# Kernel tuning notes

Measured on AMD Instinct MI355X. Metric: run time of the kernel, lower is better.

The kernel has to match this reference:

```python
import jax, jax.numpy as jnp
import numpy as np

DIM = 1024
N_HEADS = 16
HEAD_DIM = DIM // N_HEADS
MAX_SEQ_LEN = 8192
THETA = 10000.0
EPS = 1e-6


def _rope_tables(seq_len):
    freqs = 1.0 / (THETA ** (jnp.arange(0, HEAD_DIM, 2, dtype=jnp.float32) / HEAD_DIM))
    t = jnp.arange(seq_len, dtype=jnp.float32)
    ang = jnp.outer(t, freqs)  # [S, HEAD_DIM/2]
    return jnp.cos(ang), jnp.sin(ang)


def _apply_rope(x, cos, sin):
    # x: [B, H, S, hd]; cos/sin: [S, hd/2] broadcast over B,H
    x1 = x[..., ::2]
    x2 = x[..., 1::2]
    r1 = x1 * cos - x2 * sin
    r2 = x1 * sin + x2 * cos
    # interleave back: stack on last dim then flatten
    return jnp.stack([r1, r2], axis=-1).reshape(x.shape)


def _rms_norm(x, w, eps=EPS):
    dt = x.dtype
    xf = x.astype(jnp.float32)
    rms = jax.lax.rsqrt(jnp.mean(xf * xf, axis=-1, keepdims=True) + eps)
    return (xf * rms).astype(dt) * w.astype(dt)


def setup_inputs() -> dict:
    key = jax.random.key(0)
    ks = jax.random.split(key, 6)
    s = 0.02
    return {
        "x": jax.random.normal(ks[0], (2, 2048, DIM), dtype=jnp.float32),
        "Wq": jax.random.normal(ks[1], (DIM, DIM), dtype=jnp.float32) * s,
        "Wk": jax.random.normal(ks[2], (HEAD_DIM, DIM), dtype=jnp.float32) * s,
        "Wv": jax.random.normal(ks[3], (HEAD_DIM, DIM), dtype=jnp.float32) * s,
        "Wo": jax.random.normal(ks[4], (DIM, DIM), dtype=jnp.float32) * s,
        "norm_w": jnp.ones((DIM,), dtype=jnp.float32),
    }


def reference(x, Wq, Wk, Wv, Wo, norm_w):
    B, S, D = x.shape
    scale = HEAD_DIM ** -0.5
    # projections (nn.Linear: x @ W.T)
    q = (x @ Wq.T).reshape(B, S, N_HEADS, HEAD_DIM).transpose(0, 2, 1, 3)  # [B,H,S,hd]
    k = (x @ Wk.T).reshape(B, S, 1, HEAD_DIM).transpose(0, 2, 1, 3)       # [B,1,S,hd]
    v = (x @ Wv.T).reshape(B, S, 1, HEAD_DIM).transpose(0, 2, 1, 3)       # [B,1,S,hd]
    cos, sin = _rope_tables(S)
    q = _apply_rope(q, cos, sin)
    k = _apply_rope(k, cos, sin)
    # MQA: single KV head broadcast across query heads (keep k/v un-expanded)
    scores = jnp.einsum("bhqd,bzkd->bhqk", q, k) * scale  # [B,H,S,S]
    causal = jnp.tril(jnp.ones((S, S), dtype=bool))
    scores = jnp.where(causal, scores, jnp.finfo(scores.dtype).min)
    attn = jax.nn.softmax(scores, axis=-1)
    out = jnp.einsum("bhqk,bzkd->bhqd", attn, v)  # [B,H,S,hd]
    out = out.transpose(0, 2, 1, 3).reshape(B, S, D)
    out = _rms_norm(out, norm_w)
    return out @ Wo.T
```

## Files before the change

kernel.cpp:

```cpp
#include <hip/hip_runtime.h>
#include <hip/hip_bf16.h>

typedef __attribute__((ext_vector_type(4)))  float f32x4;
typedef __attribute__((ext_vector_type(16))) float f32x16;
typedef __attribute__((ext_vector_type(8)))  short s16x8;
typedef __attribute__((ext_vector_type(4)))  unsigned int u32x4;

using bf16 = __hip_bfloat16;

#define DIMC   1024
#define NH     16
#define HD     64
#define SEQ    2048
#define NB     2
#define NROWS  (NB*SEQ)
#define NQKV   1152
#define QSCL   0.18033688f

__global__ __launch_bounds__(256) void cast_all_kernel(const float* __restrict__ x,
                                                       const float* __restrict__ wq,
                                                       const float* __restrict__ wk,
                                                       const float* __restrict__ wv,
                                                       const float* __restrict__ wo,
                                                       const float* __restrict__ nw,
                                                       bf16* __restrict__ xbf,
                                                       bf16* __restrict__ wqkv,
                                                       bf16* __restrict__ wob) {
  int i = blockIdx.x * blockDim.x + threadIdx.x;
  if (i >= 1343488) {
    int j = i - 1343488;
    const float* s = wo + (size_t)j * 4;
    bf16* d = wob + (size_t)j * 4;
    int d0 = (j * 4) & 1023;
    float4 v = *(const float4*)s;
    float4 g = *(const float4*)(nw + d0);
    d[0] = __float2bfloat16(v.x * g.x);
    d[1] = __float2bfloat16(v.y * g.y);
    d[2] = __float2bfloat16(v.z * g.z);
    d[3] = __float2bfloat16(v.w * g.w);
    return;
  }
  const float* s;
  bf16* d;
  if (i < 1048576)      { s = x  + (size_t)i * 4;                 d = xbf + (size_t)i * 4; }
  else if (i < 1310720) { int j = i - 1048576; s = wq + (size_t)j * 4; d = wqkv + (size_t)j * 4; }
  else if (i < 1327104) { int j = i - 1310720; s = wk + (size_t)j * 4; d = wqkv + (size_t)1024 * 1024 + (size_t)j * 4; }
  else                  { int j = i - 1327104; s = wv + (size_t)j * 4; d = wqkv + (size_t)1088 * 1024 + (size_t)j * 4; }
  float4 v = *(const float4*)s;
  d[0] = __float2bfloat16(v.x);
  d[1] = __float2bfloat16(v.y);
  d[2] = __float2bfloat16(v.z);
  d[3] = __float2bfloat16(v.w);
}

template <bool SCALE, bool OUTBF>
__global__ __launch_bounds__(256) void gemm_bt(const bf16* __restrict__ A,
                                               const bf16* __restrict__ Bm,
                                               void* __restrict__ Cv,
                                               const float* __restrict__ ssq,
                                               int M, int N, int K) {
  __shared__ bf16 lA[128 * 64];
  __shared__ bf16 lB[64 * 64];
  __shared__ float rms_l[128];
  const int tid = threadIdx.x;
  const int w = tid >> 6, l = tid & 63;
  const int lg = l >> 4, ln = l & 15;
  const int wr = w >> 1, wc = w & 1;
  const int m0 = blockIdx.x * 128, n0 = blockIdx.y * 64;

  if (SCALE && tid < 128) {
    const float4* s4 = (const float4*)(ssq + (size_t)(m0 + tid) * 16);
    float4 a = s4[0], b = s4[1], c = s4[2], d = s4[3];
    float tot = (a.x + a.y + a.z + a.w) + (b.x + b.y + b.z + b.w) +
                (c.x + c.y + c.z + c.w) + (d.x + d.y + d.z + d.w);
    rms_l[tid] = rsqrtf(tot * (1.0f / 1024.0f) + 1e-6f);
  }

  f32x4 acc[4][2] = {};

  for (int k0 = 0; k0 < K; k0 += 64) {
#pragma unroll
    for (int it = 0; it < 4; ++it) {
      int c = tid + it * 256;
      int row = c >> 3, col = (c & 7) * 8;
      __builtin_amdgcn_global_load_lds(
          (const __attribute__((address_space(1))) void*)(A + (size_t)(m0 + row) * K + k0 + col),
          (__attribute__((address_space(3))) void*)(&lA[c * 8]), 16, 0, 0);
    }
#pragma unroll
    for (int it = 0; it < 2; ++it) {
      int c = tid + it * 256;
      int row = c >> 3, col = (c & 7) * 8;
      __builtin_amdgcn_global_load_lds(
          (const __attribute__((address_space(1))) void*)(Bm + (size_t)(n0 + row) * K + k0 + col),
          (__attribute__((address_space(3))) void*)(&lB[c * 8]), 16, 0, 0);
    }
    __syncthreads();
    for (int ks = 0; ks < 2; ++ks) {
      s16x8 af[4], bfr[2];
      for (int m = 0; m < 4; ++m)
        af[m] = *(const s16x8*)(&lA[(wr * 64 + m * 16 + ln) * 64 + ks * 32 + lg * 8]);
      for (int n = 0; n < 2; ++n)
        bfr[n] = *(const s16x8*)(&lB[(wc * 32 + n * 16 + ln) * 64 + ks * 32 + lg * 8]);
      for (int m = 0; m < 4; ++m)
        for (int n = 0; n < 2; ++n)
          acc[m][n] = __builtin_amdgcn_mfma_f32_16x16x32_bf16(af[m], bfr[n], acc[m][n], 0, 0, 0);
    }
    __syncthreads();
  }

  for (int m = 0; m < 4; ++m)
    for (int r = 0; r < 4; ++r) {
      int lrow = wr * 64 + m * 16 + lg * 4 + r;
      int grow = m0 + lrow;
      float sc = SCALE ? rms_l[lrow] : 1.0f;
      for (int n = 0; n < 2; ++n) {
        float v = SCALE ? acc[m][n][r] * sc : acc[m][n][r];
        size_t idx = (size_t)grow * N + n0 + wc * 32 + n * 16 + ln;
        if (OUTBF) ((bf16*)Cv)[idx] = __float2bfloat16(v);
        else       ((float*)Cv)[idx] = v;
      }
    }
}

__global__ __launch_bounds__(256) void rope_kernel(const bf16* __restrict__ Y,
                                                   bf16* __restrict__ QF,
                                                   bf16* __restrict__ KF,
                                                   bf16* __restrict__ VF) {
  const int r = blockIdx.x;
  const int b = r >> 11, s = r & 2047;
  const int qt = s >> 5, ql = s & 31;
  const bf16* y = Y + (size_t)r * NQKV;
  for (int t = threadIdx.x; t < 576; t += blockDim.x) {
    if (t < 512) {
      int h = t >> 5, i = t & 31;
      float x1 = __bfloat162float(y[h * 64 + 2 * i]);
      float x2 = __bfloat162float(y[h * 64 + 2 * i + 1]);
      float fr = expf(-(float)i * (9.210340371976184f / 32.0f));
      float sn, cs;
      sincosf((float)s * fr, &sn, &cs);
      int f = 2 * i;
      int ks = f >> 4, hi = (f >> 3) & 1, j = f & 7;
      bf16* q = QF + ((size_t)((((b * NH + h) * 64 + qt) * 4 + ks) * 64 + hi * 32 + ql)) * 8 + j;
      q[0] = __float2bfloat16((x1 * cs - x2 * sn) * QSCL);
      q[1] = __float2bfloat16((x1 * sn + x2 * cs) * QSCL);
    } else if (t < 544) {
      int i = t - 512;
      float x1 = __bfloat162float(y[1024 + 2 * i]);
      float x2 = __bfloat162float(y[1024 + 2 * i + 1]);
      float fr = expf(-(float)i * (9.210340371976184f / 32.0f));
      float sn, cs;
      sincosf((float)s * fr, &sn, &cs);
      int f = 2 * i;
      int ks = f >> 4, hi = (f >> 3) & 1, j = f & 7;
      bf16* k = KF + ((size_t)(((b * 64 + qt) * 4 + ks) * 64 + hi * 32 + ql)) * 8 + j;
      k[0] = __float2bfloat16(x1 * cs - x2 * sn);
      k[1] = __float2bfloat16(x1 * sn + x2 * cs);
    } else {
      int i = t - 544;
      int d0 = 2 * i;
      int c = (s >> 4) & 1, hv = (s >> 3) & 1, jv = s & 7;
      int dt = d0 >> 5;
      bf16* p0 = VF + ((size_t)((((b * 64 + qt) * 2 + c) * 2 + dt) * 64 + hv * 32 + (d0 & 31))) * 8 + jv;
      p0[0] = y[1088 + d0];
      p0[8] = y[1088 + d0 + 1];
    }
  }
}

static __device__ __forceinline__ unsigned cvt_pk_bf16(float lo, float hi) {
  unsigned r;
  asm("v_cvt_pk_bf16_f32 %0, %1, %2" : "=v"(r) : "v"(lo), "v"(hi));
  return r;
}
static __device__ __forceinline__ void pl32_swap(unsigned& x, unsigned& y) {
  asm("v_permlane32_swap_b32 %0, %1" : "+v"(x), "+v"(y));
}

__global__ __launch_bounds__(256, 2) void attn12_kernel(const bf16* __restrict__ QF,
                                                        const bf16* __restrict__ KF,
                                                        const bf16* __restrict__ VF,
                                                        bf16* __restrict__ Nb,
                                                        float* __restrict__ ssq) {
  __shared__ float cb[2][64][66];
  const int bid = blockIdx.x;
  const int fold = bid >> 4;
  const int hp = (bid >> 1) & 7;
  const int b  = bid & 1;
  const int w  = threadIdx.x >> 6;
  const int l  = threadIdx.x & 63;
  const int ql = l & 31, hi = l >> 5;
  const int h0 = hp * 2, h1 = hp * 2 + 1;

  auto run_qtile = [&](int qt) {
    const bf16* qp0 = QF + ((size_t)((b * NH + h0) * 64 + qt) * 256 + l) * 8;
    const bf16* qp1 = QF + ((size_t)((b * NH + h1) * 64 + qt) * 256 + l) * 8;
    s16x8 qf0[4], qf1[4];
#pragma unroll
    for (int ks = 0; ks < 4; ++ks) {
      qf0[ks] = *(const s16x8*)(qp0 + ks * 512);
      qf1[ks] = *(const s16x8*)(qp1 + ks * 512);
    }

    const bf16* kp = KF + ((size_t)(b * 64 + w) * 256 + l) * 8;
    const bf16* vp = VF + ((size_t)(b * 64 + w) * 256 + l) * 8;

    f32x16 ot0[2] = {}, ot1[2] = {};
    float ls0 = 0.f, ls1 = 0.f;

    auto loadK = [&](s16x8 (&kf)[4]) {
#pragma unroll
      for (int ks = 0; ks < 4; ++ks) kf[ks] = *(const s16x8*)(kp + ks * 512);
      kp += 4 * 1024 * 2;
    };

    auto softmax_pv = [&](const f32x16& sa, const f32x16& sb, bool diag,
                          float& ls, f32x16 (&ot)[2], s16x8 (&vf)[4]) {
      float p[16];
      if (diag) {
#pragma unroll
        for (int r = 0; r < 16; ++r) {
          const int cr = (r & 3) + 8 * (r >> 2);
          p[r] = (cr + 4 * hi > ql) ? 0.f : exp2f(sa[r] + sb[r]);
        }
      } else {
#pragma unroll
        for (int r = 0; r < 16; ++r) p[r] = exp2f(sa[r] + sb[r]);
      }
      float t8[8];
#pragma unroll
      for (int r = 0; r < 8; ++r) t8[r] = p[2 * r] + p[2 * r + 1];
#pragma unroll
      for (int r = 0; r < 4; ++r) t8[r] = t8[r] + t8[r + 4];
      float rs = (t8[0] + t8[2]) + (t8[1] + t8[3]);
      rs += __shfl_xor(rs, 32);
      ls += rs;
#pragma unroll
      for (int c = 0; c < 2; ++c) {
        unsigned w0 = cvt_pk_bf16(p[c * 8 + 0], p[c * 8 + 1]);
        unsigned w2 = cvt_pk_bf16(p[c * 8 + 4], p[c * 8 + 5]);
        unsigned w1 = cvt_pk_bf16(p[c * 8 + 2], p[c * 8 + 3]);
        unsigned w3 = cvt_pk_bf16(p[c * 8 + 6], p[c * 8 + 7]);
        pl32_swap(w0, w2);
        pl32_swap(w1, w3);
        u32x4 pu = {w0, w1, w2, w3};
        s16x8 pb = *(s16x8*)&pu;
        __builtin_amdgcn_s_setprio(1);
#pragma unroll
        for (int dt = 0; dt < 2; ++dt)
          ot[dt] = __builtin_amdgcn_mfma_f32_32x32x16_bf16(vf[c * 2 + dt], pb, ot[dt], 0, 0, 0);
        __builtin_amdgcn_s_setprio(0);
      }
    };

    auto compute = [&](int t, s16x8 (&kf)[4]) {
      s16x8 vf[4];
#pragma unroll
      for (int j = 0; j < 4; ++j) vf[j] = *(const s16x8*)(vp + j * 512);
      vp += 4 * 1024 * 2;
      const bool diag = (t == qt);
      f32x16 s0a = {}, s0b = {}, s1a = {}, s1b = {};
      __builtin_amdgcn_s_setprio(1);
      s0a = __builtin_amdgcn_mfma_f32_32x32x16_bf16(kf[0], qf0[0], s0a, 0, 0, 0);
      s1a = __builtin_amdgcn_mfma_f32_32x32x16_bf16(kf[0], qf1[0], s1a, 0, 0, 0);
      s0b = __builtin_amdgcn_mfma_f32_32x32x16_bf16(kf[2], qf0[2], s0b, 0, 0, 0);
      s1b = __builtin_amdgcn_mfma_f32_32x32x16_bf16(kf[2], qf1[2], s1b, 0, 0, 0);
      s0a = __builtin_amdgcn_mfma_f32_32x32x16_bf16(kf[1], qf0[1], s0a, 0, 0, 0);
      s1a = __builtin_amdgcn_mfma_f32_32x32x16_bf16(kf[1], qf1[1], s1a, 0, 0, 0);
      s0b = __builtin_amdgcn_mfma_f32_32x32x16_bf16(kf[3], qf0[3], s0b, 0, 0, 0);
      s1b = __builtin_amdgcn_mfma_f32_32x32x16_bf16(kf[3], qf1[3], s1b, 0, 0, 0);
      __builtin_amdgcn_s_setprio(0);
      softmax_pv(s0a, s0b, diag, ls0, ot0, vf);
      softmax_pv(s1a, s1b, diag, ls1, ot1, vf);
    };

    s16x8 kA[4], kB[4];
    int t = w;
    if (t <= qt) {
      loadK(kA);
      while (true) {
        if (t + 4 <= qt) loadK(kB);
        compute(t, kA);
        t += 4;
        if (t > qt) break;
        if (t + 4 <= qt) loadK(kA);
        compute(t, kB);
        t += 4;
        if (t > qt) break;
      }
    }

    auto dumpLDS = [&](int slot) {
      float* dst = &cb[slot][l][0];
#pragma unroll
      for (int r = 0; r < 16; ++r) {
        dst[r]      = ot0[0][r];
        dst[16 + r] = ot0[1][r];
        dst[32 + r] = ot1[0][r];
        dst[48 + r] = ot1[1][r];
      }
      dst[64] = ls0; dst[65] = ls1;
    };
    auto mergeLDS = [&](int slot) {
      const float* src = &cb[slot][l][0];
#pragma unroll
      for (int r = 0; r < 16; ++r) {
        ot0[0][r] += src[r];
        ot0[1][r] += src[16 + r];
        ot1[0][r] += src[32 + r];
        ot1[1][r] += src[48 + r];
      }
      ls0 += src[64]; ls1 += src[65];
    };

    __syncthreads();
    if (w == 1) dumpLDS(0);
    if (w == 3) dumpLDS(1);
    __syncthreads();
    if (w == 0) mergeLDS(0);
    if (w == 2) mergeLDS(1);
    __syncthreads();
    if (w == 2) dumpLDS(0);
    __syncthreads();
    if (w == 0) {
      mergeLDS(0);
      const int rowg = b * SEQ + qt * 32 + ql;
      {
        float inv = 1.0f / ls0;
        float sq = 0.f;
        bf16* nb = Nb + (size_t)rowg * DIMC + h0 * HD;
#pragma unroll
        for (int dt = 0; dt < 2; ++dt)
#pragma unroll
          for (int rq = 0; rq < 4; ++rq) {
            float o0 = ot0[dt][4 * rq + 0] * inv, o1 = ot0[dt][4 * rq + 1] * inv;
            float o2 = ot0[dt][4 * rq + 2] * inv, o3 = ot0[dt][4 * rq + 3] * inv;
            sq += o0 * o0 + o1 * o1 + o2 * o2 + o3 * o3;
            uint2 pk = { cvt_pk_bf16(o0, o1), cvt_pk_bf16(o2, o3) };
            *(uint2*)(nb + dt * 32 + rq * 8 + 4 * hi) = pk;
          }
        sq += __shfl_xor(sq, 32);
        if (hi == 0) ssq[rowg * 16 + h0] = sq;
      }
      {
        float inv = 1.0f / ls1;
        float sq = 0.f;
        bf16* nb = Nb + (size_t)rowg * DIMC + h1 * HD;
#pragma unroll
        for (int dt = 0; dt < 2; ++dt)
#pragma unroll
          for (int rq = 0; rq < 4; ++rq) {
            float o0 = ot1[dt][4 * rq + 0] * inv, o1 = ot1[dt][4 * rq + 1] * inv;
            float o2 = ot1[dt][4 * rq + 2] * inv, o3 = ot1[dt][4 * rq + 3] * inv;
            sq += o0 * o0 + o1 * o1 + o2 * o2 + o3 * o3;
            uint2 pk = { cvt_pk_bf16(o0, o1), cvt_pk_bf16(o2, o3) };
            *(uint2*)(nb + dt * 32 + rq * 8 + 4 * hi) = pk;
          }
        sq += __shfl_xor(sq, 32);
        if (hi == 0) ssq[rowg * 16 + h1] = sq;
      }
    }
  };

  run_qtile(fold);
  run_qtile(63 - fold);
}

extern "C" void kernel_launch(void* const* d_in, const int* in_sizes, int n_in,
                              void* d_out, int out_size, void* d_ws, size_t ws_size,
                              hipStream_t stream) {
  const float* x      = (const float*)d_in[0];
  const float* Wq     = (const float*)d_in[1];
  const float* Wk     = (const float*)d_in[2];
  const float* Wv     = (const float*)d_in[3];
  const float* Wo     = (const float*)d_in[4];
  const float* norm_w = (const float*)d_in[5];

  size_t off = 0;
  auto alloc = [&](size_t bytes) {
    void* p = (char*)d_ws + off;
    off += (bytes + 255) & ~(size_t)255;
    return p;
  };
  bf16*  Xbf  = (bf16*)alloc((size_t)NROWS * DIMC * 2);
  bf16*  Wqkv = (bf16*)alloc((size_t)NQKV * DIMC * 2);
  bf16*  Wob  = (bf16*)alloc((size_t)DIMC * DIMC * 2);
  bf16*  Yb   = (bf16*)alloc((size_t)NROWS * NQKV * 2);
  bf16*  QF   = (bf16*)alloc((size_t)NB * NH * 64 * 4 * 64 * 8 * 2);
  bf16*  KF   = (bf16*)alloc((size_t)NB * 64 * 4 * 64 * 8 * 2);
  bf16*  VF   = (bf16*)alloc((size_t)NB * 64 * 4 * 64 * 8 * 2);
  bf16*  Nb   = (bf16*)alloc((size_t)NROWS * DIMC * 2);
  float* ssq  = (float*)alloc((size_t)NROWS * 16 * 4);

  cast_all_kernel<<<6272, 256, 0, stream>>>(x, Wq, Wk, Wv, Wo, norm_w, Xbf, Wqkv, Wob);

  gemm_bt<false, true><<<dim3(NROWS / 128, NQKV / 64), 256, 0, stream>>>(
      Xbf, Wqkv, Yb, nullptr, NROWS, NQKV, DIMC);

  rope_kernel<<<NROWS, 256, 0, stream>>>(Yb, QF, KF, VF);

  attn12_kernel<<<NB * 8 * 32, 256, 0, stream>>>(QF, KF, VF, Nb, ssq);

  gemm_bt<true, false><<<dim3(NROWS / 128, DIMC / 64), 256, 0, stream>>>(
      Nb, Wob, (float*)d_out, ssq, NROWS, DIMC, DIMC);
}
```

Measured before the change: 102.2 us.

## Double-buffer GEMM LDS tiles and swizzle block order across XCDs

```diff
diff --git a/kernel.cpp b/kernel.cpp
--- a/kernel.cpp
+++ b/kernel.cpp
@@ -59,14 +59,19 @@
                                                void* __restrict__ Cv,
                                                const float* __restrict__ ssq,
                                                int M, int N, int K) {
-  __shared__ bf16 lA[128 * 64];
-  __shared__ bf16 lB[64 * 64];
+  __shared__ bf16 lA[2][128 * 64];
+  __shared__ bf16 lB[2][64 * 64];
   __shared__ float rms_l[128];
   const int tid = threadIdx.x;
   const int w = tid >> 6, l = tid & 63;
   const int lg = l >> 4, ln = l & 15;
   const int wr = w >> 1, wc = w & 1;
-  const int m0 = blockIdx.x * 128, n0 = blockIdx.y * 64;
+
+  const int nm = M >> 7;
+  const int nwg = gridDim.x;
+  const int bid = blockIdx.x;
+  const int swz = (bid & 7) * (nwg >> 3) + (bid >> 3);
+  const int m0 = (swz % nm) * 128, n0 = (swz / nm) * 64;
 
   if (SCALE && tid < 128) {
     const float4* s4 = (const float4*)(ssq + (size_t)(m0 + tid) * 16);
@@ -76,16 +81,14 @@
     rms_l[tid] = rsqrtf(tot * (1.0f / 1024.0f) + 1e-6f);
   }
 
-  f32x4 acc[4][2] = {};
-
-  for (int k0 = 0; k0 < K; k0 += 64) {
+  auto stage = [&](int buf, int k0) {
 #pragma unroll
     for (int it = 0; it < 4; ++it) {
       int c = tid + it * 256;
       int row = c >> 3, col = (c & 7) * 8;
       __builtin_amdgcn_global_load_lds(
           (const __attribute__((address_space(1))) void*)(A + (size_t)(m0 + row) * K + k0 + col),
-          (__attribute__((address_space(3))) void*)(&lA[c * 8]), 16, 0, 0);
+          (__attribute__((address_space(3))) void*)(&lA[buf][c * 8]), 16, 0, 0);
     }
 #pragma unroll
     for (int it = 0; it < 2; ++it) {
@@ -93,20 +96,42 @@
       int row = c >> 3, col = (c & 7) * 8;
       __builtin_amdgcn_global_load_lds(
           (const __attribute__((address_space(1))) void*)(Bm + (size_t)(n0 + row) * K + k0 + col),
-          (__attribute__((address_space(3))) void*)(&lB[c * 8]), 16, 0, 0);
-    }
-    __syncthreads();
+          (__attribute__((address_space(3))) void*)(&lB[buf][c * 8]), 16, 0, 0);
+    }
+  };
+
+  f32x4 acc[4][2] = {};
+
+  stage(0, 0);
+  int cur = 0;
+  const int NS = K >> 6;
+  for (int s = 0; s < NS; ++s) {
+    if (s + 1 < NS) {
+      stage(cur ^ 1, (s + 1) << 6);
+      asm volatile("s_waitcnt vmcnt(6)");
+    } else {
+      asm volatile("s_waitcnt vmcnt(0)");
+    }
+    __builtin_amdgcn_s_barrier();
+    __builtin_amdgcn_sched_barrier(0);
+#pragma unroll
     for (int ks = 0; ks < 2; ++ks) {
       s16x8 af[4], bfr[2];
+#pragma unroll
       for (int m = 0; m < 4; ++m)
-        af[m] = *(const s16x8*)(&lA[(wr * 64 + m * 16 + ln) * 64 + ks * 32 + lg * 8]);
+        af[m] = *(const s16x8*)(&lA[cur][(wr * 64 + m * 16 + ln) * 64 + ks * 32 + lg * 8]);
+#pragma unroll
       for (int n = 0; n < 2; ++n)
-        bfr[n] = *(const s16x8*)(&lB[(wc * 32 + n * 16 + ln) * 64 + ks * 32 + lg * 8]);
+        bfr[n] = *(const s16x8*)(&lB[cur][(wc * 32 + n * 16 + ln) * 64 + ks * 32 + lg * 8]);
+#pragma unroll
       for (int m = 0; m < 4; ++m)
+#pragma unroll
         for (int n = 0; n < 2; ++n)
           acc[m][n] = __builtin_amdgcn_mfma_f32_16x16x32_bf16(af[m], bfr[n], acc[m][n], 0, 0, 0);
     }
-    __syncthreads();
+    __builtin_amdgcn_sched_barrier(0);
+    __builtin_amdgcn_s_barrier();
+    cur ^= 1;
   }
 
   for (int m = 0; m < 4; ++m)
@@ -394,13 +419,13 @@
 
   cast_all_kernel<<<6272, 256, 0, stream>>>(x, Wq, Wk, Wv, Wo, norm_w, Xbf, Wqkv, Wob);
 
-  gemm_bt<false, true><<<dim3(NROWS / 128, NQKV / 64), 256, 0, stream>>>(
+  gemm_bt<false, true><<<(NROWS / 128) * (NQKV / 64), 256, 0, stream>>>(
       Xbf, Wqkv, Yb, nullptr, NROWS, NQKV, DIMC);
 
   rope_kernel<<<NROWS, 256, 0, stream>>>(Yb, QF, KF, VF);
 
   attn12_kernel<<<NB * 8 * 32, 256, 0, stream>>>(QF, KF, VF, Nb, ssq);
 
-  gemm_bt<true, false><<<dim3(NROWS / 128, DIMC / 64), 256, 0, stream>>>(
+  gemm_bt<true, false><<<(NROWS / 128) * (DIMC / 64), 256, 0, stream>>>(
       Nb, Wob, (float*)d_out, ssq, NROWS, DIMC, DIMC);
 }
```

After: 106.2 us. 1.04x slower.

## Fuse RoPE and QKV layout scatter into the QKV GEMM epilogue

Applied to the files above, without the earlier changes.

```diff
diff --git a/kernel.cpp b/kernel.cpp
--- a/kernel.cpp
+++ b/kernel.cpp
@@ -25,8 +25,18 @@
                                                        const float* __restrict__ nw,
                                                        bf16* __restrict__ xbf,
                                                        bf16* __restrict__ wqkv,
-                                                       bf16* __restrict__ wob) {
+                                                       bf16* __restrict__ wob,
+                                                       float2* __restrict__ tbl) {
   int i = blockIdx.x * blockDim.x + threadIdx.x;
+  if (i >= 1605632) {
+    int idx = i - 1605632;
+    int s2 = idx >> 5, i2 = idx & 31;
+    float fr = expf(-(float)i2 * (9.210340371976184f / 32.0f));
+    float sn, cs;
+    sincosf((float)s2 * fr, &sn, &cs);
+    tbl[idx] = make_float2(cs, sn);
+    return;
+  }
   if (i >= 1343488) {
     int j = i - 1343488;
     const float* s = wo + (size_t)j * 4;
@@ -53,11 +63,15 @@
   d[3] = __float2bfloat16(v.w);
 }
 
-template <bool SCALE, bool OUTBF>
+template <int MODE>
 __global__ __launch_bounds__(256) void gemm_bt(const bf16* __restrict__ A,
                                                const bf16* __restrict__ Bm,
-                                               void* __restrict__ Cv,
+                                               float* __restrict__ C,
                                                const float* __restrict__ ssq,
+                                               bf16* __restrict__ QF,
+                                               bf16* __restrict__ KF,
+                                               bf16* __restrict__ VF,
+                                               const float2* __restrict__ tbl,
                                                int M, int N, int K) {
   __shared__ bf16 lA[128 * 64];
   __shared__ bf16 lB[64 * 64];
@@ -68,7 +82,7 @@
   const int wr = w >> 1, wc = w & 1;
   const int m0 = blockIdx.x * 128, n0 = blockIdx.y * 64;
 
-  if (SCALE && tid < 128) {
+  if (MODE == 2 && tid < 128) {
     const float4* s4 = (const float4*)(ssq + (size_t)(m0 + tid) * 16);
     float4 a = s4[0], b = s4[1], c = s4[2], d = s4[3];
     float tot = (a.x + a.y + a.z + a.w) + (b.x + b.y + b.z + b.w) +
@@ -109,62 +123,47 @@
     __syncthreads();
   }
 
-  for (int m = 0; m < 4; ++m)
-    for (int r = 0; r < 4; ++r) {
-      int lrow = wr * 64 + m * 16 + lg * 4 + r;
-      int grow = m0 + lrow;
-      float sc = SCALE ? rms_l[lrow] : 1.0f;
-      for (int n = 0; n < 2; ++n) {
-        float v = SCALE ? acc[m][n][r] * sc : acc[m][n][r];
-        size_t idx = (size_t)grow * N + n0 + wc * 32 + n * 16 + ln;
-        if (OUTBF) ((bf16*)Cv)[idx] = __float2bfloat16(v);
-        else       ((float*)Cv)[idx] = v;
-      }
-    }
-}
-
-__global__ __launch_bounds__(256) void rope_kernel(const bf16* __restrict__ Y,
-                                                   bf16* __restrict__ QF,
-                                                   bf16* __restrict__ KF,
-                                                   bf16* __restrict__ VF) {
-  const int r = blockIdx.x;
-  const int b = r >> 11, s = r & 2047;
-  const int qt = s >> 5, ql = s & 31;
-  const bf16* y = Y + (size_t)r * NQKV;
-  for (int t = threadIdx.x; t < 576; t += blockDim.x) {
-    if (t < 512) {
-      int h = t >> 5, i = t & 31;
-      float x1 = __bfloat162float(y[h * 64 + 2 * i]);
-      float x2 = __bfloat162float(y[h * 64 + 2 * i + 1]);
-      float fr = expf(-(float)i * (9.210340371976184f / 32.0f));
-      float sn, cs;
-      sincosf((float)s * fr, &sn, &cs);
-      int f = 2 * i;
-      int ks = f >> 4, hi = (f >> 3) & 1, j = f & 7;
-      bf16* q = QF + ((size_t)((((b * NH + h) * 64 + qt) * 4 + ks) * 64 + hi * 32 + ql)) * 8 + j;
-      q[0] = __float2bfloat16((x1 * cs - x2 * sn) * QSCL);
-      q[1] = __float2bfloat16((x1 * sn + x2 * cs) * QSCL);
-    } else if (t < 544) {
-      int i = t - 512;
-      float x1 = __bfloat162float(y[1024 + 2 * i]);
-      float x2 = __bfloat162float(y[1024 + 2 * i + 1]);
-      float fr = expf(-(float)i * (9.210340371976184f / 32.0f));
-      float sn, cs;
-      sincosf((float)s * fr, &sn, &cs);
-      int f = 2 * i;
-      int ks = f >> 4, hi = (f >> 3) & 1, j = f & 7;
-      bf16* k = KF + ((size_t)(((b * 64 + qt) * 4 + ks) * 64 + hi * 32 + ql)) * 8 + j;
-      k[0] = __float2bfloat16(x1 * cs - x2 * sn);
-      k[1] = __float2bfloat16(x1 * sn + x2 * cs);
-    } else {
-      int i = t - 544;
-      int d0 = 2 * i;
-      int c = (s >> 4) & 1, hv = (s >> 3) & 1, jv = s & 7;
-      int dt = d0 >> 5;
-      bf16* p0 = VF + ((size_t)((((b * 64 + qt) * 2 + c) * 2 + dt) * 64 + hv * 32 + (d0 & 31))) * 8 + jv;
-      p0[0] = y[1088 + d0];
-      p0[8] = y[1088 + d0 + 1];
-    }
+  if (MODE == 1) {
+    const int by = blockIdx.y;
+#pragma unroll
+    for (int m = 0; m < 4; ++m)
+#pragma unroll
+      for (int r = 0; r < 4; ++r) {
+        int row = m0 + wr * 64 + m * 16 + lg * 4 + r;
+        int b2 = row >> 11, s2 = row & 2047;
+        int qt = s2 >> 5, ql2 = s2 & 31;
+#pragma unroll
+        for (int n = 0; n < 2; ++n) {
+          float v = acc[m][n][r];
+          int f = wc * 32 + n * 16 + ln;
+          if (by < 17) {
+            float p = __shfl_xor(v, 1);
+            float2 cs2 = tbl[(size_t)s2 * 32 + (f >> 1)];
+            float rot = (ln & 1) ? fmaf(p, cs2.y, v * cs2.x)
+                                 : fmaf(v, cs2.x, -p * cs2.y);
+            int ks2 = f >> 4, hi2 = (f >> 3) & 1, j2 = f & 7;
+            if (by < 16)
+              QF[(((((size_t)b2 * NH + by) * 64 + qt) * 4 + ks2) * 64 + hi2 * 32 + ql2) * 8 + j2] =
+                  __float2bfloat16(rot * QSCL);
+            else
+              KF[((((size_t)b2 * 64 + qt) * 4 + ks2) * 64 + hi2 * 32 + ql2) * 8 + j2] =
+                  __float2bfloat16(rot);
+          } else {
+            int c2 = (s2 >> 4) & 1, hv = (s2 >> 3) & 1, jv = s2 & 7, dt = f >> 5;
+            VF[(((((size_t)b2 * 64 + qt) * 2 + c2) * 2 + dt) * 64 + hv * 32 + (f & 31)) * 8 + jv] =
+                __float2bfloat16(v);
+          }
+        }
+      }
+  } else {
+    for (int m = 0; m < 4; ++m)
+      for (int r = 0; r < 4; ++r) {
+        int lrow = wr * 64 + m * 16 + lg * 4 + r;
+        int grow = m0 + lrow;
+        float sc = rms_l[lrow];
+        for (int n = 0; n < 2; ++n)
+          C[(size_t)grow * N + n0 + wc * 32 + n * 16 + ln] = acc[m][n][r] * sc;
+      }
   }
 }
 
@@ -211,7 +210,7 @@
     auto loadK = [&](s16x8 (&kf)[4]) {
 #pragma unroll
       for (int ks = 0; ks < 4; ++ks) kf[ks] = *(const s16x8*)(kp + ks * 512);
-      kp += 4 * 1024 * 2;
+      kp += 4 * 2048;
     };
 
     auto softmax_pv = [&](const f32x16& sa, const f32x16& sb, bool diag,
@@ -257,7 +256,7 @@
       s16x8 vf[4];
 #pragma unroll
       for (int j = 0; j < 4; ++j) vf[j] = *(const s16x8*)(vp + j * 512);
-      vp += 4 * 1024 * 2;
+      vp += 4 * 2048;
       const bool diag = (t == qt);
       f32x16 s0a = {}, s0b = {}, s1a = {}, s1b = {};
       __builtin_amdgcn_s_setprio(1);
@@ -382,25 +381,25 @@
     off += (bytes + 255) & ~(size_t)255;
     return p;
   };
-  bf16*  Xbf  = (bf16*)alloc((size_t)NROWS * DIMC * 2);
-  bf16*  Wqkv = (bf16*)alloc((size_t)NQKV * DIMC * 2);
-  bf16*  Wob  = (bf16*)alloc((size_t)DIMC * DIMC * 2);
-  bf16*  Yb   = (bf16*)alloc((size_t)NROWS * NQKV * 2);
-  bf16*  QF   = (bf16*)alloc((size_t)NB * NH * 64 * 4 * 64 * 8 * 2);
-  bf16*  KF   = (bf16*)alloc((size_t)NB * 64 * 4 * 64 * 8 * 2);
-  bf16*  VF   = (bf16*)alloc((size_t)NB * 64 * 4 * 64 * 8 * 2);
-  bf16*  Nb   = (bf16*)alloc((size_t)NROWS * DIMC * 2);
-  float* ssq  = (float*)alloc((size_t)NROWS * 16 * 4);
-
-  cast_all_kernel<<<6272, 256, 0, stream>>>(x, Wq, Wk, Wv, Wo, norm_w, Xbf, Wqkv, Wob);
-
-  gemm_bt<false, true><<<dim3(NROWS / 128, NQKV / 64), 256, 0, stream>>>(
-      Xbf, Wqkv, Yb, nullptr, NROWS, NQKV, DIMC);
-
-  rope_kernel<<<NROWS, 256, 0, stream>>>(Yb, QF, KF, VF);
+  bf16*   Xbf  = (bf16*)alloc((size_t)NROWS * DIMC * 2);
+  bf16*   Wqkv = (bf16*)alloc((size_t)NQKV * DIMC * 2);
+  bf16*   Wob  = (bf16*)alloc((size_t)DIMC * DIMC * 2);
+  bf16*   QF   = (bf16*)alloc((size_t)NB * NH * 64 * 4 * 64 * 8 * 2);
+  bf16*   KF   = (bf16*)alloc((size_t)NB * 64 * 4 * 64 * 8 * 2);
+  bf16*   VF   = (bf16*)alloc((size_t)NB * 64 * 4 * 64 * 8 * 2);
+  bf16*   Nb   = (bf16*)alloc((size_t)NROWS * DIMC * 2);
+  float*  ssq  = (float*)alloc((size_t)NROWS * 16 * 4);
+  float2* tbl  = (float2*)alloc((size_t)SEQ * 32 * 8);
+
+  cast_all_kernel<<<6528, 256, 0, stream>>>(x, Wq, Wk, Wv, Wo, norm_w,
+                                            Xbf, Wqkv, Wob, tbl);
+
+  gemm_bt<1><<<dim3(NROWS / 128, NQKV / 64), 256, 0, stream>>>(
+      Xbf, Wqkv, nullptr, nullptr, QF, KF, VF, tbl, NROWS, NQKV, DIMC);
 
   attn12_kernel<<<NB * 8 * 32, 256, 0, stream>>>(QF, KF, VF, Nb, ssq);
 
-  gemm_bt<true, false><<<dim3(NROWS / 128, DIMC / 64), 256, 0, stream>>>(
-      Nb, Wob, (float*)d_out, ssq, NROWS, DIMC, DIMC);
-}
+  gemm_bt<2><<<dim3(NROWS / 128, DIMC / 64), 256, 0, stream>>>(
+      Nb, Wob, (float*)d_out, ssq, nullptr, nullptr, nullptr, nullptr,
+      NROWS, DIMC, DIMC);
+}
```

Result: faster. 97.12 us (-5.0%).
